# Optimization experiments

Hardware: AMD Instinct MI355X
Metric: run time of the kernel (lower is better)

The kernel has to match this reference:

```python
import jax, jax.numpy as jnp
import numpy as np

DIST_SCALE = 10000.0   # divisor in kernel()
KERNEL_EPS = 0.0001    # additive epsilon before reciprocal


def setup_inputs() -> dict:
    key = jax.random.key(0)
    k1, k2, k3 = jax.random.split(key, 3)
    batch, keysize, dict_size, categories = 4096, 512, 16384, 128
    x = jax.random.normal(k1, (batch, keysize), dtype=jnp.float32)
    # keras TruncatedNormal(mean=0, stddev=3) approximated by scaled normal
    keys = 3.0 * jax.random.normal(k2, (dict_size, keysize), dtype=jnp.float32)
    V = jax.random.normal(k3, (dict_size, categories), dtype=jnp.float32)
    return {"x": x, "keys": keys, "V": V}


def reference(x, keys, V):
    # sq_distance(keys, x): (dict_size, batch)
    sq = (
        jnp.sum(keys * keys, axis=1, keepdims=True)            # (D, 1)
        - 2.0 * jnp.einsum("dk,bk->db", keys, x)               # (D, B)
        + jnp.sum(x * x, axis=1)[None, :]                      # (1, B)
    )
    kern = 1.0 / (sq / DIST_SCALE + KERNEL_EPS)                # (D, B)
    KV = jnp.einsum("db,dc->bc", kern, V)                      # (B, C)
    # original: diag(1 / (KV @ ones)) @ KV  ==  row-normalize by row sum
    return KV / jnp.sum(KV, axis=1, keepdims=True)
```

## Files before the change

kernel.cpp:

```cpp
#include <hip/hip_runtime.h>

#define BATCH 4096
#define DICT  16384
#define KDIM  512
#define CAT   128
#define ND    16
#define DSLICE (DICT/ND)
#define DCH   128
#define BT    128

typedef __attribute__((ext_vector_type(4)))  float f32x4;
typedef __attribute__((ext_vector_type(16))) float f32x16;
typedef __attribute__((ext_vector_type(8)))  short short8;
typedef __attribute__((ext_vector_type(8)))  unsigned short ushort8;
typedef __attribute__((ext_vector_type(4)))  int intx4;

__device__ __forceinline__ unsigned short f2bf(float f) {
  unsigned int u = __float_as_uint(f);
  return (unsigned short)((u + 0x7fffu + ((u >> 16) & 1u)) >> 16);
}

__device__ __forceinline__ unsigned int cvtpk_bf16(float lo, float hi) {
  unsigned int r;
  asm volatile("v_cvt_pk_bf16_f32 %0, %1, %2" : "=v"(r) : "v"(lo), "v"(hi));
  return r;
}

__device__ __forceinline__ void pl32swap(unsigned int& a, unsigned int& b) {
  asm volatile("v_permlane32_swap_b32 %0, %1" : "+v"(a), "+v"(b));
}

#define AS1 __attribute__((address_space(1)))
#define AS3 __attribute__((address_space(3)))
__device__ __forceinline__ void gl_lds16(const void* g, void* l) {
  __builtin_amdgcn_global_load_lds((AS1 void*)(g), (AS3 void*)(l), 16, 0, 0);
}

#define MFMA32(a, b, c) __builtin_amdgcn_mfma_f32_32x32x16_bf16((a), (b), (c), 0, 0, 0)

__global__ void prep_rows(const float* __restrict__ in,
                          unsigned short* __restrict__ ob,
                          float* __restrict__ sums) {
  const int lane = threadIdx.x & 63, wv = threadIdx.x >> 6;
  const int row = blockIdx.x * 4 + wv;
  const float* rp = in + ((size_t)row << 9);
  float4 a = *(const float4*)(rp + lane * 8);
  float4 b = *(const float4*)(rp + lane * 8 + 4);
  float s = a.x*a.x + a.y*a.y + a.z*a.z + a.w*a.w
          + b.x*b.x + b.y*b.y + b.z*b.z + b.w*b.w;
  ushort8 o;
  o[0]=f2bf(a.x); o[1]=f2bf(a.y); o[2]=f2bf(a.z); o[3]=f2bf(a.w);
  o[4]=f2bf(b.x); o[5]=f2bf(b.y); o[6]=f2bf(b.z); o[7]=f2bf(b.w);
  *(ushort8*)(ob + ((size_t)row << 9) + lane * 8) = o;
  #pragma unroll
  for (int m = 32; m; m >>= 1) s += __shfl_xor(s, m);
  if (lane == 0) sums[row] = s;
}

__global__ void prep_vt(const float* __restrict__ V,
                        unsigned short* __restrict__ Vt) {
  __shared__ float t[64][129];
  const int d0 = blockIdx.x * 64;
  const int tid = threadIdx.x;
  #pragma unroll
  for (int j = 0; j < 32; ++j) {
    int idx = j * 256 + tid;
    t[idx >> 7][idx & 127] = V[((size_t)d0 << 7) + idx];
  }
  __syncthreads();
  #pragma unroll
  for (int j = 0; j < 32; ++j) {
    int idx = j * 256 + tid;
    int cc = idx >> 6, dd = idx & 63;
    Vt[((size_t)cc << 14) + d0 + dd] = f2bf(t[dd][cc]);
  }
}

__global__ __launch_bounds__(256, 2)
void varkeys_fused(const unsigned short* __restrict__ xb,
                   const unsigned short* __restrict__ kb,
                   const unsigned short* __restrict__ vt,
                   const float* __restrict__ sx,
                   const float* __restrict__ sk,
                   float* __restrict__ kvp) {
  __shared__ __attribute__((aligned(16))) char lds[69632];
  char* const As = lds;
  char* const Bs = lds + 16384;
  char* const Vs = lds + 32768;
  float* const sks = (float*)(lds + 65536);

  const int tid = threadIdx.x;
  const int lane = tid & 63, r31 = lane & 31, h = lane >> 5;
  const int wv = tid >> 6;
  const int dw = wv >> 1, bw = wv & 1;

  const int bid = blockIdx.x;
  const int btile = bid & 31, dslice = bid >> 5;
  const int b0 = btile * BT;
  const int dbase = dslice * DSLICE;

  { f32x4 v = *(const f32x4*)(sk + dbase + tid * 4);
    *(f32x4*)(sks + tid * 4) = v; }
  const float sxv0 = sx[b0 + bw * 64 + r31];
  const float sxv1 = sx[b0 + bw * 64 + 32 + r31];

  const int sex   = (tid & 15) ^ (tid >> 4);
  const int srow  = 2 * (tid >> 4) + (sex >> 3);
  const int skoff = (sex & 7) << 4;
  const size_t ksrc_t = (size_t)srow * 1024 + skoff;
  const size_t vsrc_t = (size_t)srow * 32768 + skoff;

  const int MH = (((r31 & 1) << 3) | h) ^ (r31 >> 1);
  int T[4];
  #pragma unroll
  for (int ks = 0; ks < 4; ++ks) T[ks] = ((ks << 1) ^ MH) << 4;
  const int arb = (dw * 32 + (r31 >> 1)) * 256;
  const int brb = (bw * 32 + (r31 >> 1)) * 256;
  const int vrb = (r31 >> 1) * 256;

  const char* xbB = (const char*)xb;
  const char* kbB = (const char*)kb;
  const char* vtB = (const char*)vt;

  const f32x16 z16 = {0.f};
  f32x16 acc[2][4];
  #pragma unroll
  for (int j = 0; j < 2; ++j)
    #pragma unroll
    for (int n = 0; n < 4; ++n) acc[j][n] = z16;

  for (int dc = 0; dc < DSLICE / DCH; ++dc) {
    const int dg0 = dbase + dc * DCH;
    f32x16 S00 = z16, S01 = z16, S10 = z16, S11 = z16;

    for (int kk = 0; kk < KDIM / 64; ++kk) {
      __syncthreads();
      const size_t ksrc = (size_t)dg0 * 1024 + (size_t)(kk * 128) + ksrc_t;
      const size_t xsrc = (size_t)b0 * 1024 + (size_t)(kk * 128) + ksrc_t;
      #pragma unroll
      for (int p = 0; p < 4; ++p) {
        gl_lds16(kbB + ksrc + (size_t)p * 32768, As + p * 4096 + wv * 1024);
        gl_lds16(xbB + xsrc + (size_t)p * 32768, Bs + p * 4096 + wv * 1024);
      }
      if (kk >= 4) {
        #pragma unroll
        for (int t = 0; t < 2; ++t) {
          const int rr = (kk - 4) * 2 + t;
          const int hv = rr >> 2, cg = rr & 3;
          const size_t vsrc = (size_t)(cg * 32) * 32768
                            + (size_t)(dg0 + hv * 64) * 2 + vsrc_t;
          gl_lds16(vtB + vsrc, Vs + rr * 4096 + wv * 1024);
        }
      }
      __syncthreads();
      #pragma unroll
      for (int ks = 0; ks < 4; ++ks) {
        short8 a0  = *(const short8*)(As + arb + T[ks]);
        short8 a1  = *(const short8*)(As + arb + 4096 + T[ks]);
        short8 bf0 = *(const short8*)(Bs + brb + T[ks]);
        short8 bf1 = *(const short8*)(Bs + brb + 4096 + T[ks]);
        S00 = MFMA32(a0, bf0, S00);
        S01 = MFMA32(a0, bf1, S01);
        S10 = MFMA32(a1, bf0, S10);
        S11 = MFMA32(a1, bf1, S11);
      }
    }

    const float* sksb = sks + dc * DCH + dw * 64 + h * 4;
    #pragma unroll
    for (int tl = 0; tl < 4; ++tl) {
      const int i = tl >> 1, c2 = tl & 1;
      short8 pa[2];
      #pragma unroll
      for (int j = 0; j < 2; ++j) {
        const f32x16 Sv = (i == 0) ? (j == 0 ? S00 : S01) : (j == 0 ? S10 : S11);
        const float sxv = j ? sxv1 : sxv0;
        float kq[8];
        #pragma unroll
        for (int q2 = 0; q2 < 2; ++q2) {
          const int q = c2 * 2 + q2;
          const f32x4 skv = *(const f32x4*)(sksb + i * 32 + q * 8);
          #pragma unroll
          for (int rr = 0; rr < 4; ++rr)
            kq[q2 * 4 + rr] =
              10000.f * __builtin_amdgcn_rcpf(skv[rr] + sxv - 2.f * Sv[q * 4 + rr] + 1.f);
        }
        unsigned int X = cvtpk_bf16(kq[0], kq[1]);
        unsigned int Z = cvtpk_bf16(kq[2], kq[3]);
        unsigned int Y = cvtpk_bf16(kq[4], kq[5]);
        unsigned int W = cvtpk_bf16(kq[6], kq[7]);
        pl32swap(X, Y);
        pl32swap(Z, W);
        intx4 fw; fw[0] = (int)X; fw[1] = (int)Z; fw[2] = (int)Y; fw[3] = (int)W;
        pa[j] = *(short8*)&fw;
      }
      #pragma unroll
      for (int n = 0; n < 4; ++n) {
        short8 vb = *(const short8*)(Vs + dw * 16384 + n * 4096 + vrb + T[tl]);
        acc[0][n] = MFMA32(pa[0], vb, acc[0][n]);
        acc[1][n] = MFMA32(pa[1], vb, acc[1][n]);
      }
    }
  }

  __syncthreads();
  if (dw == 1) {
    #pragma unroll
    for (int j = 0; j < 2; ++j)
      #pragma unroll
      for (int n = 0; n < 4; ++n)
        #pragma unroll
        for (int s = 0; s < 4; ++s) {
          f32x4 t;
          t[0] = acc[j][n][s*4+0]; t[1] = acc[j][n][s*4+1];
          t[2] = acc[j][n][s*4+2]; t[3] = acc[j][n][s*4+3];
          *(f32x4*)(lds + bw * 32768 + ((j * 4 + n) * 4 + s) * 1024 + lane * 16) = t;
        }
  }
  __syncthreads();
  if (dw == 0) {
    #pragma unroll
    for (int j = 0; j < 2; ++j)
      #pragma unroll
      for (int n = 0; n < 4; ++n)
        #pragma unroll
        for (int s = 0; s < 4; ++s) {
          f32x4 t = *(const f32x4*)(lds + bw * 32768 + ((j * 4 + n) * 4 + s) * 1024 + lane * 16);
          acc[j][n][s*4+0] += t[0]; acc[j][n][s*4+1] += t[1];
          acc[j][n][s*4+2] += t[2]; acc[j][n][s*4+3] += t[3];
        }
    float* op = kvp + (((size_t)(dslice * BATCH + b0 + bw * 64)) << 7);
    #pragma unroll
    for (int j = 0; j < 2; ++j)
      #pragma unroll
      for (int n = 0; n < 4; ++n)
        #pragma unroll
        for (int r = 0; r < 16; ++r) {
          int row = j * 32 + (r & 3) + 8 * (r >> 2) + 4 * h;
          op[((size_t)row << 7) + n * 32 + r31] = acc[j][n][r];
        }
  }
}

__global__ void reduce_norm(const float* __restrict__ part, float* __restrict__ out) {
  const int lane = threadIdx.x & 63, wv = threadIdx.x >> 6;
  const int b = blockIdx.x * 4 + wv;
  float v0 = 0.f, v1 = 0.f;
  #pragma unroll
  for (int s = 0; s < ND; ++s) {
    const float* p = part + ((((size_t)s << 12) + b) << 7);
    v0 += p[lane]; v1 += p[lane + 64];
  }
  float t = v0 + v1;
  #pragma unroll
  for (int m = 32; m; m >>= 1) t += __shfl_xor(t, m);
  out[((size_t)b << 7) + lane]      = v0 / t;
  out[((size_t)b << 7) + lane + 64] = v1 / t;
}

extern "C" void kernel_launch(void* const* d_in, const int* in_sizes, int n_in,
                              void* d_out, int out_size, void* d_ws, size_t ws_size,
                              hipStream_t stream) {
  (void)in_sizes; (void)n_in; (void)out_size; (void)ws_size;
  const float* x    = (const float*)d_in[0];
  const float* keys = (const float*)d_in[1];
  const float* V    = (const float*)d_in[2];
  float* out = (float*)d_out;
  char* ws = (char*)d_ws;
  unsigned short* xb = (unsigned short*)(ws);
  unsigned short* kb = (unsigned short*)(ws + ((size_t)4 << 20));
  unsigned short* vt = (unsigned short*)(ws + ((size_t)20 << 20));
  float* sx  = (float*)(ws + ((size_t)24 << 20));
  float* sk  = (float*)(ws + ((size_t)24 << 20) + (1 << 16));
  float* kvp = (float*)(ws + ((size_t)25 << 20));

  prep_rows<<<BATCH / 4, 256, 0, stream>>>(x, xb, sx);
  prep_rows<<<DICT / 4, 256, 0, stream>>>(keys, kb, sk);
  prep_vt<<<DICT / 64, 256, 0, stream>>>(V, vt);
  varkeys_fused<<<32 * ND, 256, 0, stream>>>(xb, kb, vt, sx, sk, kvp);
  reduce_norm<<<BATCH / 4, 256, 0, stream>>>(kvp, out);
}
```

Baseline: 161.6 us.

## Double-buffer A/B tiles with vmcnt waits and widen batch tile to 256

The fused distance-kernel-matmul now uses 512-thread blocks covering 256 batch rows, which halves the number of blocks and doubles reuse of each key tile. Global-to-LDS loads of the key/x tiles are double-buffered and prefetched one k-step ahead, synchronised with explicit s_waitcnt vmcnt and raw s_barrier instead of two __syncthreads per step. Squared key norms are loaded into registers instead of being staged in LDS. The cost is a 128KB LDS footprint and fewer blocks (256), which may hurt occupancy. The epilogue section that is not shown may still assume the old 4-wave layout.

New measurement: 244.8 us. 51.5% more time.

```diff
diff --git a/kernel.cpp b/kernel.cpp
--- a/kernel.cpp
+++ b/kernel.cpp
@@ -7,7 +7,7 @@
 #define ND    16
 #define DSLICE (DICT/ND)
 #define DCH   128
-#define BT    128
+#define BT    256
 
 typedef __attribute__((ext_vector_type(4)))  float f32x4;
 typedef __attribute__((ext_vector_type(16))) float f32x16;
@@ -34,6 +34,14 @@
 #define AS3 __attribute__((address_space(3)))
 __device__ __forceinline__ void gl_lds16(const void* g, void* l) {
   __builtin_amdgcn_global_load_lds((AS1 void*)(g), (AS3 void*)(l), 16, 0, 0);
+}
+
+template <int N>
+__device__ __forceinline__ void waitv() {
+  if constexpr (N == 0)      asm volatile("s_waitcnt vmcnt(0)" ::: "memory");
+  else if constexpr (N == 6) asm volatile("s_waitcnt vmcnt(6)" ::: "memory");
+  else                       asm volatile("s_waitcnt vmcnt(7)" ::: "memory");
+  __builtin_amdgcn_sched_barrier(0);
 }
 
 #define MFMA32(a, b, c) __builtin_amdgcn_mfma_f32_32x32x16_bf16((a), (b), (c), 0, 0, 0)
@@ -76,39 +84,28 @@
   }
 }
 
-__global__ __launch_bounds__(256, 2)
+__global__ __launch_bounds__(512, 2)
 void varkeys_fused(const unsigned short* __restrict__ xb,
                    const unsigned short* __restrict__ kb,
                    const unsigned short* __restrict__ vt,
                    const float* __restrict__ sx,
                    const float* __restrict__ sk,
                    float* __restrict__ kvp) {
-  __shared__ __attribute__((aligned(16))) char lds[69632];
-  char* const As = lds;
-  char* const Bs = lds + 16384;
-  char* const Vs = lds + 32768;
-  float* const sks = (float*)(lds + 65536);
+  __shared__ __attribute__((aligned(16))) char lds[131072];
+  char* const VsB = lds + 98304;
 
   const int tid = threadIdx.x;
   const int lane = tid & 63, r31 = lane & 31, h = lane >> 5;
   const int wv = tid >> 6;
-  const int dw = wv >> 1, bw = wv & 1;
+  const int dw = wv >> 2, bw = wv & 3;
 
   const int bid = blockIdx.x;
-  const int btile = bid & 31, dslice = bid >> 5;
+  const int btile = bid & 15, dslice = bid >> 4;
   const int b0 = btile * BT;
   const int dbase = dslice * DSLICE;
 
-  { f32x4 v = *(const f32x4*)(sk + dbase + tid * 4);
-    *(f32x4*)(sks + tid * 4) = v; }
   const float sxv0 = sx[b0 + bw * 64 + r31];
   const float sxv1 = sx[b0 + bw * 64 + 32 + r31];
-
-  const int sex   = (tid & 15) ^ (tid >> 4);
-  const int srow  = 2 * (tid >> 4) + (sex >> 3);
-  const int skoff = (sex & 7) << 4;
-  const size_t ksrc_t = (size_t)srow * 1024 + skoff;
-  const size_t vsrc_t = (size_t)srow * 32768 + skoff;
 
   const int MH = (((r31 & 1) << 3) | h) ^ (r31 >> 1);
   int T[4];
@@ -129,30 +126,65 @@
     #pragma unroll
     for (int n = 0; n < 4; ++n) acc[j][n] = z16;
 
+  auto stageAB = [&](int ns) {
+    const int dg2 = dbase + (ns >> 3) * DCH;
+    const int kb2 = (ns & 7) << 7;
+    char* A2 = lds + (ns & 1) * 16384;
+    char* B2 = lds + 32768 + (ns & 1) * 32768;
+    #pragma unroll
+    for (int r = 0; r < 2; ++r) {
+      const int L = r * 8192 + tid * 16;
+      const int pr = L >> 8, g = ((L >> 4) & 15) ^ (pr & 15);
+      gl_lds16(kbB + ((size_t)(dg2 + 2 * pr + (g >> 3)) << 10) + kb2 + ((g & 7) << 4),
+               A2 + r * 8192 + wv * 1024);
+    }
+    #pragma unroll
+    for (int r = 0; r < 4; ++r) {
+      const int L = r * 8192 + tid * 16;
+      const int pr = L >> 8, g = ((L >> 4) & 15) ^ (pr & 15);
+      gl_lds16(xbB + ((size_t)(b0 + 2 * pr + (g >> 3)) << 10) + kb2 + ((g & 7) << 4),
+               B2 + r * 8192 + wv * 1024);
+    }
+  };
+
+  stageAB(0);
+
+  f32x4 skq[2][4];
+
   for (int dc = 0; dc < DSLICE / DCH; ++dc) {
-    const int dg0 = dbase + dc * DCH;
+    const int dg = dbase + dc * DCH;
     f32x16 S00 = z16, S01 = z16, S10 = z16, S11 = z16;
 
-    for (int kk = 0; kk < KDIM / 64; ++kk) {
-      __syncthreads();
-      const size_t ksrc = (size_t)dg0 * 1024 + (size_t)(kk * 128) + ksrc_t;
-      const size_t xsrc = (size_t)b0 * 1024 + (size_t)(kk * 128) + ksrc_t;
-      #pragma unroll
-      for (int p = 0; p < 4; ++p) {
-        gl_lds16(kbB + ksrc + (size_t)p * 32768, As + p * 4096 + wv * 1024);
-        gl_lds16(xbB + xsrc + (size_t)p * 32768, Bs + p * 4096 + wv * 1024);
-      }
-      if (kk >= 4) {
-        #pragma unroll
-        for (int t = 0; t < 2; ++t) {
-          const int rr = (kk - 4) * 2 + t;
-          const int hv = rr >> 2, cg = rr & 3;
-          const size_t vsrc = (size_t)(cg * 32) * 32768
-                            + (size_t)(dg0 + hv * 64) * 2 + vsrc_t;
-          gl_lds16(vtB + vsrc, Vs + rr * 4096 + wv * 1024);
-        }
-      }
-      __syncthreads();
+    #pragma unroll
+    for (int kk = 0; kk < 8; ++kk) {
+      __builtin_amdgcn_s_barrier();
+      if (kk == 0) {
+        #pragma unroll
+        for (int i = 0; i < 2; ++i)
+          #pragma unroll
+          for (int q = 0; q < 4; ++q)
+            skq[i][q] = *(const f32x4*)(sk + dg + dw * 64 + i * 32 + q * 8 + h * 4);
+      }
+      const int ns = dc * 8 + kk + 1;
+      if (ns < 64) stageAB(ns);
+      if (kk >= 2 && kk <= 5) {
+        const int vr = kk - 2;
+        const int L = vr * 8192 + tid * 16;
+        const int rr = L >> 12, l = L & 4095;
+        const int pr = l >> 8, g = ((l >> 4) & 15) ^ pr;
+        const int c = (rr & 3) * 32 + 2 * pr + (g >> 3);
+        gl_lds16(vtB + ((size_t)c << 15) + ((size_t)(dg + (rr >> 2) * 64) << 1)
+                     + ((g & 7) << 4),
+                 VsB + vr * 8192 + wv * 1024);
+      }
+      if (ns == 64) waitv<0>();
+      else if (kk >= 2 && kk <= 5) waitv<7>();
+      else waitv<6>();
+      __builtin_amdgcn_s_barrier();
+      __builtin_amdgcn_sched_barrier(0);
+
+      const char* As = lds + (kk & 1) * 16384;
+      const char* Bs = lds + 32768 + (kk & 1) * 32768;
       #pragma unroll
       for (int ks = 0; ks < 4; ++ks) {
         short8 a0  = *(const short8*)(As + arb + T[ks]);
@@ -166,7 +198,6 @@
       }
     }
 
-    const float* sksb = sks + dc * DCH + dw * 64 + h * 4;
     #pragma unroll
     for (int tl = 0; tl < 4; ++tl) {
       const int i = tl >> 1, c2 = tl & 1;
@@ -179,7 +210,7 @@
         #pragma unroll
         for (int q2 = 0; q2 < 2; ++q2) {
           const int q = c2 * 2 + q2;
-          const f32x4 skv = *(const f32x4*)(sksb + i * 32 + q * 8);
+          const f32x4 skv = skq[i][q];
           #pragma unroll
           for (int rr = 0; rr < 4; ++rr)
             kq[q2 * 4 + rr] =
@@ -196,7 +227,7 @@
       }
       #pragma unroll
       for (int n = 0; n < 4; ++n) {
-        short8 vb = *(const short8*)(Vs + dw * 16384 + n * 4096 + vrb + T[tl]);
+        short8 vb = *(const short8*)(VsB + dw * 16384 + n * 4096 + vrb + T[tl]);
         acc[0][n] = MFMA32(pa[0], vb, acc[0][n]);
         acc[1][n] = MFMA32(pa[1], vb, acc[1][n]);
       }
@@ -277,6 +308,6 @@
   prep_rows<<<BATCH / 4, 256, 0, stream>>>(x, xb, sx);
   prep_rows<<<DICT / 4, 256, 0, stream>>>(keys, kb, sk);
   prep_vt<<<DICT / 64, 256, 0, stream>>>(V, vt);
-  varkeys_fused<<<32 * ND, 256, 0, stream>>>(xb, kb, vt, sx, sk, kvp);
+  varkeys_fused<<<(BATCH / BT) * ND, 512, 0, stream>>>(xb, kb, vt, sx, sk, kvp);
   reduce_norm<<<BATCH / 4, 256, 0, stream>>>(kvp, out);
 }
```
